# Kernel optimization log

Hardware: AMD Instinct MI355X
Metric: run time of the kernel (lower is better)

## Reference

```python
import jax, jax.numpy as jnp
import numpy as np

N_NODES = 100000
N_EDGES = 1700000  # 1.6M random edges + 100k self-loops (dgl.add_self_loop)
HID = 128
N_GRAPHS = 64
N_CLASSES = 10
T_STEPS = 5


def setup_inputs() -> dict:
    key = jax.random.key(0)
    ks = jax.random.split(key, 12)
    m = jax.random.normal(ks[0], (N_NODES,), dtype=jnp.float32)
    n_rand = N_EDGES - N_NODES
    src_r = jax.random.randint(ks[1], (n_rand,), 0, N_NODES)
    dst_r = jax.random.randint(ks[2], (n_rand,), 0, N_NODES)
    loops = jnp.arange(N_NODES)
    src = jnp.concatenate([src_r, loops])
    dst = jnp.concatenate([dst_r, loops])
    graph_ids = jnp.sort(jax.random.randint(ks[3], (N_NODES,), 0, N_GRAPHS))
    s = 0.05
    W_e = jax.random.normal(ks[4], (HID, HID), dtype=jnp.float32) * s
    b_e = jnp.zeros((HID,), dtype=jnp.float32)
    W_ih = jax.random.normal(ks[5], (3 * HID, HID), dtype=jnp.float32) * s
    b_ih = jnp.zeros((3 * HID,), dtype=jnp.float32)
    W_hh = jax.random.normal(ks[6], (3 * HID, HID), dtype=jnp.float32) * s
    b_hh = jnp.zeros((3 * HID,), dtype=jnp.float32)
    W_cls = jax.random.normal(ks[7], (N_CLASSES, HID), dtype=jnp.float32) * s
    b_cls = jnp.zeros((N_CLASSES,), dtype=jnp.float32)
    return {"m": m, "W_e": W_e, "b_e": b_e, "W_ih": W_ih, "b_ih": b_ih,
            "W_hh": W_hh, "b_hh": b_hh, "W_cls": W_cls, "b_cls": b_cls,
            "src": src, "dst": dst, "graph_ids": graph_ids, "n_graphs": N_GRAPHS}


def _gated_graph_forward(m, W_e, b_e, W_ih, b_ih, W_hh, b_hh, W_cls, b_cls,
                         src, dst, graph_ids, n_graphs):
    n_nodes = m.shape[0]
    hid = W_e.shape[0]
    # h = ndata['m'].view(-1,1), zero-padded to out_feats (DGL GatedGraphConv)
    h = jnp.zeros((n_nodes, hid), dtype=m.dtype).at[:, 0].set(m)
    for _ in range(T_STEPS):
        # single edge type: a[v] = sum_{(u,v) in E} W_e h[u] + b_e
        msg = (h @ W_e.T + b_e)[src]                       # [E, H]
        a = jax.ops.segment_sum(msg, dst, num_segments=n_nodes)
        # torch.nn.GRUCell(a, h); gate order: r, z, n
        gi = a @ W_ih.T + b_ih
        gh = h @ W_hh.T + b_hh
        i_r, i_z, i_n = jnp.split(gi, 3, axis=-1)
        h_r, h_z, h_n = jnp.split(gh, 3, axis=-1)
        r = jax.nn.sigmoid(i_r + h_r)
        z = jax.nn.sigmoid(i_z + h_z)
        n = jnp.tanh(i_n + r * h_n)
        h = (1.0 - z) * n + z * h
    h = jax.nn.relu(h)
    # dgl.mean_nodes: per-graph mean over nodes
    sums = jax.ops.segment_sum(h, graph_ids, num_segments=n_graphs)
    cnt = jax.ops.segment_sum(jnp.ones((n_nodes,), h.dtype), graph_ids,
                              num_segments=n_graphs)
    hg = sums / jnp.maximum(cnt, 1.0)[:, None]             # [G, H]
    return hg @ W_cls.T + b_cls                            # [G, C]


def reference(m, W_e, b_e, W_ih, b_ih, W_hh, b_hh, W_cls, b_cls,
              src, dst, graph_ids, n_graphs):
    return _gated_graph_forward(m, W_e, b_e, W_ih, b_ih, W_hh, b_hh,
                                W_cls, b_cls, src, dst, graph_ids, n_graphs)
```

## Files before the change

kernel.cpp:

```cpp
#include <hip/hip_runtime.h>

#define HID 128
#define G3  384
#define TSTEPS 5
#define BSHIFT 9
#define BNODES (1 << BSHIFT)
#define MAXBUK 256
#define PART_EPB 8192

typedef unsigned int  uint;
typedef unsigned short ushort;

typedef float  f32x4  __attribute__((ext_vector_type(4)));
typedef __bf16 bf16x8 __attribute__((ext_vector_type(8)));

union B8u { uint4 u; bf16x8 b; ushort s[8]; };

static __device__ inline ushort f2bf(float f) {
  uint u = __float_as_uint(f);
  uint r = u + 0x7fffu + ((u >> 16) & 1u);
  return (ushort)(r >> 16);
}
static __device__ inline float bf2f(ushort s) {
  return __uint_as_float(((uint)s) << 16);
}

__global__ __launch_bounds__(128) void k_weights(
    const float* __restrict__ W_e, const float* __restrict__ b_e,
    const float* __restrict__ W_ih, const float* __restrict__ W_hh,
    ushort* __restrict__ Wcomb, ushort* __restrict__ Whh16, float* __restrict__ bvec,
    ushort* __restrict__ Wc0, ushort* __restrict__ Wh0)
{
  int j = blockIdx.x, t = threadIdx.x;
  if (j < G3) {
    __shared__ float row[HID];
    row[t] = W_ih[j * HID + t];
    __syncthreads();
    float acc = 0.f;
    for (int k = 0; k < HID; ++k) acc = fmaf(row[k], W_e[k * HID + t], acc);
    Wcomb[j * HID + t] = f2bf(acc);
    if (t == 0) {
      Wc0[j] = f2bf(acc);
      float b = 0.f;
      for (int k = 0; k < HID; ++k) b += row[k] * b_e[k];
      bvec[j] = b;
    }
  } else {
    int j2 = j - G3;
    Whh16[j2 * HID + t] = f2bf(W_hh[j2 * HID + t]);
    if (t == 0) Wh0[j2] = f2bf(W_hh[j2 * HID]);
  }
}

__global__ __launch_bounds__(256) void k_bh(const int* __restrict__ dst,
                                            int* __restrict__ bhist, int E) {
  __shared__ int lh[MAXBUK];
  int t = threadIdx.x;
  if (t < MAXBUK) lh[t] = 0;
  __syncthreads();
  for (int e = blockIdx.x * 256 + t; e < E; e += gridDim.x * 256)
    atomicAdd(&lh[dst[e] >> BSHIFT], 1);
  __syncthreads();
  if (t < MAXBUK && lh[t]) atomicAdd(&bhist[t], lh[t]);
}

__global__ __launch_bounds__(256) void k_bsc(const int* __restrict__ bhist,
                                             int* __restrict__ bbase,
                                             int* __restrict__ gcur,
                                             int* __restrict__ rowptr, int E, int N) {
  __shared__ int ls[MAXBUK];
  int t = threadIdx.x;
  ls[t] = bhist[t];
  __syncthreads();
  if (t == 0) {
    int run = 0;
    for (int i = 0; i < MAXBUK; ++i) {
      bbase[i] = run; gcur[i] = run; run += ls[i];
    }
    bbase[MAXBUK] = run;
    rowptr[N] = E;
  }
}

__global__ __launch_bounds__(256) void k_part(
    const int* __restrict__ src, const int* __restrict__ dst,
    int* __restrict__ gcur, uint* __restrict__ ebuf, int E) {
  __shared__ int lh[MAXBUK], lbase[MAXBUK], lcur[MAXBUK];
  int t = threadIdx.x;
  int base = blockIdx.x * PART_EPB;
  if (t < MAXBUK) lh[t] = 0;
  __syncthreads();
#pragma unroll 4
  for (int j = 0; j < PART_EPB / 256; ++j) {
    int e = base + j * 256 + t;
    if (e < E) atomicAdd(&lh[dst[e] >> BSHIFT], 1);
  }
  __syncthreads();
  if (t < MAXBUK) {
    lbase[t] = lh[t] ? atomicAdd(&gcur[t], lh[t]) : 0;
    lcur[t] = 0;
  }
  __syncthreads();
#pragma unroll 4
  for (int j = 0; j < PART_EPB / 256; ++j) {
    int e = base + j * 256 + t;
    if (e < E) {
      int d = dst[e];
      int b = d >> BSHIFT;
      int p = atomicAdd(&lcur[b], 1);
      ebuf[lbase[b] + p] = (uint)src[e] | ((uint)(d & (BNODES - 1)) << 20);
    }
  }
}

__global__ __launch_bounds__(256) void k_fill2(
    const uint* __restrict__ ebuf, const int* __restrict__ bbase,
    int* __restrict__ csrc, int* __restrict__ rowptr, int* __restrict__ deg, int N) {
  __shared__ int hcnt[BNODES];
  __shared__ int wls[4];
  int t = threadIdx.x;
  int b = blockIdx.x;
  int ebeg = bbase[b], eend = bbase[b + 1];
  for (int i = t; i < BNODES; i += 256) hcnt[i] = 0;
  __syncthreads();
  for (int e = ebeg + t; e < eend; e += 256)
    atomicAdd(&hcnt[ebuf[e] >> 20], 1);
  __syncthreads();
  const int PER = BNODES / 256;
  int lane = t & 63, wv = t >> 6;
  int x[PER]; int s = 0;
#pragma unroll
  for (int i = 0; i < PER; ++i) { x[i] = hcnt[PER * t + i]; s += x[i]; }
  int incl = s;
#pragma unroll
  for (int off = 1; off < 64; off <<= 1) {
    int u = __shfl_up(incl, off, 64);
    if (lane >= off) incl += u;
  }
  if (lane == 63) wls[wv] = incl;
  __syncthreads();
  int wbase = 0;
  for (int i = 0; i < wv; ++i) wbase += wls[i];
  int run = wbase + incl - s;
#pragma unroll
  for (int i = 0; i < PER; ++i) {
    int node = (b << BSHIFT) + PER * t + i;
    hcnt[PER * t + i] = run;
    if (node < N) { rowptr[node] = ebeg + run; deg[node] = x[i]; }
    run += x[i];
  }
  __syncthreads();
  for (int e = ebeg + t; e < eend; e += 256) {
    uint v = ebuf[e];
    int p = atomicAdd(&hcnt[v >> 20], 1);
    csrc[ebeg + p] = (int)(v & 0xFFFFFu);
  }
}

__global__ void k_minit(const float* __restrict__ m, ushort* __restrict__ m16, int N) {
  int v = blockIdx.x * 256 + threadIdx.x;
  if (v < N) m16[v] = f2bf(m[v]);
}

__global__ __launch_bounds__(256) void k_gather0(
    const int* __restrict__ rowptr, const int* __restrict__ csrc,
    const ushort* __restrict__ m16, ushort* __restrict__ hsum0, int N)
{
  int v = blockIdx.x * 256 + threadIdx.x;
  if (v >= N) return;
  int beg = rowptr[v], end = rowptr[v + 1];
  float a0 = 0.f, a1 = 0.f, a2 = 0.f, a3 = 0.f;
  int e = beg;
  for (; e + 16 <= end; e += 16) {
    a0 += (bf2f(m16[csrc[e + 0]]) + bf2f(m16[csrc[e + 4]])) +
          (bf2f(m16[csrc[e + 8]]) + bf2f(m16[csrc[e + 12]]));
    a1 += (bf2f(m16[csrc[e + 1]]) + bf2f(m16[csrc[e + 5]])) +
          (bf2f(m16[csrc[e + 9]]) + bf2f(m16[csrc[e + 13]]));
    a2 += (bf2f(m16[csrc[e + 2]]) + bf2f(m16[csrc[e + 6]])) +
          (bf2f(m16[csrc[e + 10]]) + bf2f(m16[csrc[e + 14]]));
    a3 += (bf2f(m16[csrc[e + 3]]) + bf2f(m16[csrc[e + 7]])) +
          (bf2f(m16[csrc[e + 11]]) + bf2f(m16[csrc[e + 15]]));
  }
  for (; e < end; e += 4) {
    if (e + 0 < end) a0 += bf2f(m16[csrc[e + 0]]);
    if (e + 1 < end) a1 += bf2f(m16[csrc[e + 1]]);
    if (e + 2 < end) a2 += bf2f(m16[csrc[e + 2]]);
    if (e + 3 < end) a3 += bf2f(m16[csrc[e + 3]]);
  }
  hsum0[v] = f2bf((a0 + a1) + (a2 + a3));
}

__global__ __launch_bounds__(256) void k_gru0(
    const ushort* __restrict__ hsum0, const ushort* __restrict__ m16,
    const int* __restrict__ deg,
    const ushort* __restrict__ Wc0, const ushort* __restrict__ Wh0,
    const float* __restrict__ bvec, const float* __restrict__ b_ih,
    const float* __restrict__ b_hh, ushort* __restrict__ hbn, int N)
{
  int idx = blockIdx.x * 256 + threadIdx.x;
  if (idx >= N * HID) return;
  int n = idx >> 7, d = idx & (HID - 1);
  float s0 = bf2f(hsum0[n]);
  float h0 = bf2f(m16[n]);
  float degf = (float)deg[n];
  float acc0 = s0 * bf2f(Wc0[d]);
  float acc1 = s0 * bf2f(Wc0[d + 128]);
  float acc2 = s0 * bf2f(Wc0[d + 256]);
  float acc3 = h0 * bf2f(Wh0[d]);
  float acc4 = h0 * bf2f(Wh0[d + 128]);
  float acc5 = h0 * bf2f(Wh0[d + 256]);
  float hold = (d == 0) ? h0 : 0.f;
  float ir = acc0 + degf * bvec[d] + b_ih[d];
  float iz = acc1 + degf * bvec[d + 128] + b_ih[d + 128];
  float in_ = acc2 + degf * bvec[d + 256] + b_ih[d + 256];
  float hr = acc3 + b_hh[d];
  float hz = acc4 + b_hh[d + 128];
  float hn = acc5 + b_hh[d + 256];
  float r = __builtin_amdgcn_rcpf(1.f + __expf(-(ir + hr)));
  float z = __builtin_amdgcn_rcpf(1.f + __expf(-(iz + hz)));
  float x2 = in_ + r * hn;
  float e2 = __expf(2.f * x2);
  float nv = 1.f - 2.f * __builtin_amdgcn_rcpf(e2 + 1.f);
  float hv = (1.f - z) * nv + z * hold;
  hbn[idx] = f2bf(hv);
}

static __device__ __forceinline__ void gather_strip(
    const int* __restrict__ rowptr, const int* __restrict__ csrc,
    const ushort* __restrict__ hb, const int* __restrict__ deg,
    int strip, int w, int lane, int N,
    ushort dstS[16][128], ushort dstH[16][128], int* dstDeg)
{
  int node = strip * 16 + w;
  if (node >= N) return;
  int g = lane >> 4;
  int i = lane & 15;
  if (g == 1)
    *(uint4*)(&dstH[w][(i ^ (w & 7)) * 8]) =
        *(const uint4*)(hb + (size_t)node * HID + i * 8);
  if (lane == 32) dstDeg[w] = deg[node];
  int beg = rowptr[node], end = rowptr[node + 1];
  float acc[8] = {0.f, 0.f, 0.f, 0.f, 0.f, 0.f, 0.f, 0.f};
  int e = beg;
  for (; e + 16 <= end; e += 16) {
    int s0 = csrc[e + g];
    int s1 = csrc[e + 4 + g];
    int s2 = csrc[e + 8 + g];
    int s3 = csrc[e + 12 + g];
    B8u w0; w0.u = *(const uint4*)(hb + (size_t)s0 * HID + i * 8);
    B8u w1; w1.u = *(const uint4*)(hb + (size_t)s1 * HID + i * 8);
    B8u w2; w2.u = *(const uint4*)(hb + (size_t)s2 * HID + i * 8);
    B8u w3; w3.u = *(const uint4*)(hb + (size_t)s3 * HID + i * 8);
#pragma unroll
    for (int j = 0; j < 8; ++j)
      acc[j] += (bf2f(w0.s[j]) + bf2f(w1.s[j])) + (bf2f(w2.s[j]) + bf2f(w3.s[j]));
  }
  int rem = end - e;
  if (rem > 0) {
    int t0 = (g < rem)      ? csrc[e + g]      : -1;
    int t1 = (4 + g < rem)  ? csrc[e + 4 + g]  : -1;
    int t2 = (8 + g < rem)  ? csrc[e + 8 + g]  : -1;
    int t3 = (12 + g < rem) ? csrc[e + 12 + g] : -1;
    B8u r0, r1, r2, r3;
    if (t0 >= 0) r0.u = *(const uint4*)(hb + (size_t)t0 * HID + i * 8);
    if (t1 >= 0) r1.u = *(const uint4*)(hb + (size_t)t1 * HID + i * 8);
    if (t2 >= 0) r2.u = *(const uint4*)(hb + (size_t)t2 * HID + i * 8);
    if (t3 >= 0) r3.u = *(const uint4*)(hb + (size_t)t3 * HID + i * 8);
    if (t0 >= 0) {
#pragma unroll
      for (int j = 0; j < 8; ++j) acc[j] += bf2f(r0.s[j]);
    }
    if (t1 >= 0) {
#pragma unroll
      for (int j = 0; j < 8; ++j) acc[j] += bf2f(r1.s[j]);
    }
    if (t2 >= 0) {
#pragma unroll
      for (int j = 0; j < 8; ++j) acc[j] += bf2f(r2.s[j]);
    }
    if (t3 >= 0) {
#pragma unroll
      for (int j = 0; j < 8; ++j) acc[j] += bf2f(r3.s[j]);
    }
  }
#pragma unroll
  for (int j = 0; j < 8; ++j) {
    acc[j] += __shfl_xor(acc[j], 16, 64);
    acc[j] += __shfl_xor(acc[j], 32, 64);
  }
  if (g == 0) {
    uint4 ov;
    ov.x = ((uint)f2bf(acc[1]) << 16) | (uint)f2bf(acc[0]);
    ov.y = ((uint)f2bf(acc[3]) << 16) | (uint)f2bf(acc[2]);
    ov.z = ((uint)f2bf(acc[5]) << 16) | (uint)f2bf(acc[4]);
    ov.w = ((uint)f2bf(acc[7]) << 16) | (uint)f2bf(acc[6]);
    *(uint4*)(&dstS[w][(i ^ (w & 7)) * 8]) = ov;
  }
}

__global__ __launch_bounds__(1024, 4) void k_fused(
    const int* __restrict__ rowptr, const int* __restrict__ csrc,
    const ushort* __restrict__ hbc, ushort* __restrict__ hbn,
    const ushort* __restrict__ Wcomb, const ushort* __restrict__ Whh16,
    const float* __restrict__ bvec, const float* __restrict__ b_ih,
    const float* __restrict__ b_hh, const int* __restrict__ deg, int N)
{
  __shared__ float S[6][16][132];
  __shared__ ushort AT[3][2][16][128];
  __shared__ int degT[3][16];
  const int tid = threadIdx.x;
  const int w = tid >> 6;
  const int lane = tid & 63;
  const int quad = lane >> 4, l16 = lane & 15;
  const int gm = w >> 3;
  const int gw = w & 7;
  const int d0 = gw * 16;

  const ushort* Wmat = gm ? Whh16 : Wcomb;
  B8u bfr[3][4];
#pragma unroll
  for (int g = 0; g < 3; ++g)
#pragma unroll
    for (int kc = 0; kc < 4; ++kc) {
      int j = (d0 + g * 128 + l16) * HID + kc * 32 + quad * 8;
      bfr[g][kc].u = *(const uint4*)(Wmat + j);
    }

  const int ecol = tid & 127, erow0 = tid >> 7;
  const float bir = b_ih[ecol], biz = b_ih[ecol + 128], bin_ = b_ih[ecol + 256];
  const float bhr = b_hh[ecol], bhz = b_hh[ecol + 128], bhn = b_hh[ecol + 256];
  const float vr = bvec[ecol], vz = bvec[ecol + 128], vn = bvec[ecol + 256];

  const int nstrip = N >> 4;
  const int G = (int)gridDim.x;
  int s = blockIdx.x;
  if (s >= nstrip) return;

  gather_strip(rowptr, csrc, hbc, deg, s, w, lane, N, AT[0][0], AT[0][1], degT[0]);
  asm volatile("s_waitcnt lgkmcnt(0)" ::: "memory");
  __builtin_amdgcn_sched_barrier(0);
  __builtin_amdgcn_s_barrier();

  int cur = 0;
  while (true) {
    int ns = s + G;
    bool more = ns < nstrip;
    int nxt = (cur == 2) ? 0 : cur + 1;
    if (more)
      gather_strip(rowptr, csrc, hbc, deg, ns, w, lane, N,
                   AT[nxt][0], AT[nxt][1], degT[nxt]);
    B8u af[4];
#pragma unroll
    for (int kc = 0; kc < 4; ++kc)
      af[kc].u = *(const uint4*)(&AT[cur][gm][l16][(((quad + 4 * kc) ^ (l16 & 7)) * 8)]);
    f32x4 acc[3] = {};
#pragma unroll
    for (int kc = 0; kc < 4; ++kc)
#pragma unroll
      for (int g = 0; g < 3; ++g)
        acc[g] = __builtin_amdgcn_mfma_f32_16x16x32_bf16(af[kc].b, bfr[g][kc].b, acc[g], 0, 0, 0);
    __builtin_amdgcn_s_barrier();
#pragma unroll
    for (int g = 0; g < 3; ++g)
#pragma unroll
      for (int rg = 0; rg < 4; ++rg)
        S[gm * 3 + g][quad * 4 + rg][d0 + l16] = acc[g][rg];
    asm volatile("s_waitcnt lgkmcnt(0)" ::: "memory");
    __builtin_amdgcn_sched_barrier(0);
    __builtin_amdgcn_s_barrier();
    int n0 = s << 4;
#pragma unroll
    for (int k = 0; k < 2; ++k) {
      int row = erow0 + 8 * k;
      float dgf = (float)degT[cur][row];
      int sc = (((ecol >> 3) ^ (row & 7)) * 8) + (ecol & 7);
      float hold = bf2f(AT[cur][1][row][sc]);
      float ir  = S[0][row][ecol] + dgf * vr + bir;
      float iz  = S[1][row][ecol] + dgf * vz + biz;
      float in_ = S[2][row][ecol] + dgf * vn + bin_;
      float hr  = S[3][row][ecol] + bhr;
      float hz  = S[4][row][ecol] + bhz;
      float hn  = S[5][row][ecol] + bhn;
      float r = __builtin_amdgcn_rcpf(1.f + __expf(-(ir + hr)));
      float z = __builtin_amdgcn_rcpf(1.f + __expf(-(iz + hz)));
      float x2 = in_ + r * hn;
      float e2 = __expf(2.f * x2);
      float nv = 1.f - 2.f * __builtin_amdgcn_rcpf(e2 + 1.f);
      float hv = (1.f - z) * nv + z * hold;
      hbn[(size_t)(n0 + row) * HID + ecol] = f2bf(hv);
    }
    if (!more) break;
    s = ns; cur = nxt;
  }
}

__global__ __launch_bounds__(64) void k_bounds(const int* __restrict__ gid,
                                               int* __restrict__ cnt, int N, int G) {
  int g = threadIdx.x;
  if (g >= G) return;
  int lo = 0, hi = N;
  while (lo < hi) { int mid = (lo + hi) >> 1; if (gid[mid] < g) lo = mid + 1; else hi = mid; }
  int lb0 = lo;
  lo = 0; hi = N;
  int g1 = g + 1;
  while (lo < hi) { int mid = (lo + hi) >> 1; if (gid[mid] < g1) lo = mid + 1; else hi = mid; }
  cnt[g] = lo - lb0;
}

#define POOL_CHUNK 96
__global__ __launch_bounds__(128) void k_pool(const ushort* __restrict__ hb,
                                              const int* __restrict__ gid,
                                              float* __restrict__ hg, int N) {
  int d = threadIdx.x;
  int start = blockIdx.x * POOL_CHUNK;
  if (start >= N) return;
  int end = min(start + POOL_CHUNK, N);
  float acc = 0.f;
  int g = gid[start];
  for (int n = start; n < end; ++n) {
    int gn = gid[n];
    if (gn != g) { unsafeAtomicAdd(&hg[g * HID + d], acc); acc = 0.f; g = gn; }
    acc += fmaxf(bf2f(hb[(size_t)n * HID + d]), 0.f);
  }
  unsafeAtomicAdd(&hg[g * HID + d], acc);
}

__global__ __launch_bounds__(640) void k_cls(const float* __restrict__ hg,
                                             const int* __restrict__ cnt,
                                             const float* __restrict__ Wc,
                                             const float* __restrict__ bc,
                                             float* __restrict__ out, int G) {
  int t = threadIdx.x;
  if (t >= G * 10) return;
  int g = t / 10, c = t % 10;
  float inv = 1.f / fmaxf((float)cnt[g], 1.f);
  float acc = 0.f;
  for (int d = 0; d < HID; ++d) acc = fmaf(hg[g * HID + d], Wc[c * HID + d], acc);
  out[t] = acc * inv + bc[c];
}

extern "C" void kernel_launch(void* const* d_in, const int* in_sizes, int n_in,
                              void* d_out, int out_size, void* d_ws, size_t ws_size,
                              hipStream_t stream) {
  const int N = in_sizes[0];
  const int E = in_sizes[9];
  const float* m    = (const float*)d_in[0];
  const float* W_e  = (const float*)d_in[1];
  const float* b_e  = (const float*)d_in[2];
  const float* W_ih = (const float*)d_in[3];
  const float* b_ih = (const float*)d_in[4];
  const float* W_hh = (const float*)d_in[5];
  const float* b_hh = (const float*)d_in[6];
  const float* W_cls = (const float*)d_in[7];
  const float* b_cls = (const float*)d_in[8];
  const int* src = (const int*)d_in[9];
  const int* dst = (const int*)d_in[10];
  const int* gid = (const int*)d_in[11];
  const int G = out_size / 10;
  float* out = (float*)d_out;

  size_t off = 0;
  auto alloc = [&](size_t b) {
    char* p = (char*)d_ws + off;
    off += (b + 255) & ~(size_t)255;
    return (void*)p;
  };
  ushort* hb0    = (ushort*)alloc((size_t)N * HID * 2);
  ushort* hb1    = (ushort*)alloc((size_t)N * HID * 2);
  int*    deg    = (int*)   alloc((size_t)N * 4);
  int*    rowptr = (int*)   alloc((size_t)(N + 1) * 4);
  int*    csrc   = (int*)   alloc((size_t)E * 4);
  uint*   ebuf   = (uint*)  alloc((size_t)E * 4);
  int*    bhist  = (int*)   alloc((size_t)MAXBUK * 4);
  int*    bbase  = (int*)   alloc((size_t)(MAXBUK + 1) * 4);
  int*    gcur   = (int*)   alloc((size_t)MAXBUK * 4);
  ushort* Wcomb  = (ushort*)alloc((size_t)G3 * HID * 2);
  ushort* Whh16  = (ushort*)alloc((size_t)G3 * HID * 2);
  float*  bvec   = (float*) alloc((size_t)G3 * 4);
  float*  hg     = (float*) alloc((size_t)G * HID * 4);
  int*    cnt    = (int*)   alloc((size_t)G * 4);
  ushort* m16    = (ushort*)alloc((size_t)N * 2);
  ushort* hsum0  = (ushort*)alloc((size_t)N * 2);
  ushort* Wc0    = (ushort*)alloc((size_t)G3 * 2);
  ushort* Wh0    = (ushort*)alloc((size_t)G3 * 2);
  if (off > ws_size) return;

  const int NBUK = (N + BNODES - 1) >> BSHIFT;

  k_weights<<<2 * G3, HID, 0, stream>>>(W_e, b_e, W_ih, W_hh, Wcomb, Whh16, bvec, Wc0, Wh0);
  k_minit<<<(N + 255) / 256, 256, 0, stream>>>(m, m16, N);
  hipMemsetAsync(bhist, 0, (size_t)MAXBUK * 4, stream);
  k_bh<<<256, 256, 0, stream>>>(dst, bhist, E);
  k_bsc<<<1, MAXBUK, 0, stream>>>(bhist, bbase, gcur, rowptr, E, N);
  k_part<<<(E + PART_EPB - 1) / PART_EPB, 256, 0, stream>>>(src, dst, gcur, ebuf, E);
  k_fill2<<<NBUK, 256, 0, stream>>>(ebuf, bbase, csrc, rowptr, deg, N);

  k_gather0<<<(N + 255) / 256, 256, 0, stream>>>(rowptr, csrc, m16, hsum0, N);
  k_gru0<<<(N * HID + 255) / 256, 256, 0, stream>>>(hsum0, m16, deg, Wc0, Wh0,
                                                    bvec, b_ih, b_hh, hb1, N);

  ushort* hbc = hb1;
  ushort* hbn = hb0;
  const int nstrip = N >> 4;
  const int fuse_blocks = nstrip < 256 ? nstrip : 256;
  for (int s = 1; s < TSTEPS; ++s) {
    k_fused<<<fuse_blocks, 1024, 0, stream>>>(rowptr, csrc, hbc, hbn,
                                              Wcomb, Whh16, bvec, b_ih, b_hh, deg, N);
    ushort* t = hbc; hbc = hbn; hbn = t;
  }

  hipMemsetAsync(hg, 0, (size_t)G * HID * 4, stream);
  k_bounds<<<1, 64, 0, stream>>>(gid, cnt, N, G);
  k_pool<<<(N + POOL_CHUNK - 1) / POOL_CHUNK, HID, 0, stream>>>(hbc, gid, hg, N);
  k_cls<<<1, 640, 0, stream>>>(hg, cnt, W_cls, b_cls, out, G);
}
```

Measured before the change: 764.6 us.

## Prefetch neighbor indices one strip ahead and specialize gather for low degree

The fused GRU kernel now loads the CSR neighbor indices (up to 28 per node) for the strip after next while the current strip is processed. This breaks the dependent load chain rowptr→csrc→h row inside the gather. Nodes with up to 28 edges take an unrolled path that issues all row loads at once, and higher-degree nodes fall back to the generic loop. Bias vectors are moved into shared memory to free registers, at the cost of holding seven more index registers per lane under a 1024-thread launch bound.

```diff
diff --git a/kernel.cpp b/kernel.cpp
--- a/kernel.cpp
+++ b/kernel.cpp
@@ -225,6 +225,54 @@
   hbn[idx] = f2bf(hv);
 }
 
+static __device__ __forceinline__ void accum_range(
+    const ushort* __restrict__ hb, const int* __restrict__ csrc,
+    int beg, int end, int g, int i, float acc[8])
+{
+  int e = beg;
+  for (; e + 16 <= end; e += 16) {
+    int s0 = csrc[e + g];
+    int s1 = csrc[e + 4 + g];
+    int s2 = csrc[e + 8 + g];
+    int s3 = csrc[e + 12 + g];
+    B8u w0; w0.u = *(const uint4*)(hb + (size_t)s0 * HID + i * 8);
+    B8u w1; w1.u = *(const uint4*)(hb + (size_t)s1 * HID + i * 8);
+    B8u w2; w2.u = *(const uint4*)(hb + (size_t)s2 * HID + i * 8);
+    B8u w3; w3.u = *(const uint4*)(hb + (size_t)s3 * HID + i * 8);
+#pragma unroll
+    for (int j = 0; j < 8; ++j)
+      acc[j] += (bf2f(w0.s[j]) + bf2f(w1.s[j])) + (bf2f(w2.s[j]) + bf2f(w3.s[j]));
+  }
+  int rem = end - e;
+  if (rem > 0) {
+    int t0 = (g < rem)      ? csrc[e + g]      : -1;
+    int t1 = (4 + g < rem)  ? csrc[e + 4 + g]  : -1;
+    int t2 = (8 + g < rem)  ? csrc[e + 8 + g]  : -1;
+    int t3 = (12 + g < rem) ? csrc[e + 12 + g] : -1;
+    B8u r0, r1, r2, r3;
+    if (t0 >= 0) r0.u = *(const uint4*)(hb + (size_t)t0 * HID + i * 8);
+    if (t1 >= 0) r1.u = *(const uint4*)(hb + (size_t)t1 * HID + i * 8);
+    if (t2 >= 0) r2.u = *(const uint4*)(hb + (size_t)t2 * HID + i * 8);
+    if (t3 >= 0) r3.u = *(const uint4*)(hb + (size_t)t3 * HID + i * 8);
+    if (t0 >= 0) {
+#pragma unroll
+      for (int j = 0; j < 8; ++j) acc[j] += bf2f(r0.s[j]);
+    }
+    if (t1 >= 0) {
+#pragma unroll
+      for (int j = 0; j < 8; ++j) acc[j] += bf2f(r1.s[j]);
+    }
+    if (t2 >= 0) {
+#pragma unroll
+      for (int j = 0; j < 8; ++j) acc[j] += bf2f(r2.s[j]);
+    }
+    if (t3 >= 0) {
+#pragma unroll
+      for (int j = 0; j < 8; ++j) acc[j] += bf2f(r3.s[j]);
+    }
+  }
+}
+
 static __device__ __forceinline__ void gather_strip(
     const int* __restrict__ rowptr, const int* __restrict__ csrc,
     const ushort* __restrict__ hb, const int* __restrict__ deg,
@@ -241,48 +289,7 @@
   if (lane == 32) dstDeg[w] = deg[node];
   int beg = rowptr[node], end = rowptr[node + 1];
   float acc[8] = {0.f, 0.f, 0.f, 0.f, 0.f, 0.f, 0.f, 0.f};
-  int e = beg;
-  for (; e + 16 <= end; e += 16) {
-    int s0 = csrc[e + g];
-    int s1 = csrc[e + 4 + g];
-    int s2 = csrc[e + 8 + g];
-    int s3 = csrc[e + 12 + g];
-    B8u w0; w0.u = *(const uint4*)(hb + (size_t)s0 * HID + i * 8);
-    B8u w1; w1.u = *(const uint4*)(hb + (size_t)s1 * HID + i * 8);
-    B8u w2; w2.u = *(const uint4*)(hb + (size_t)s2 * HID + i * 8);
-    B8u w3; w3.u = *(const uint4*)(hb + (size_t)s3 * HID + i * 8);
-#pragma unroll
-    for (int j = 0; j < 8; ++j)
-      acc[j] += (bf2f(w0.s[j]) + bf2f(w1.s[j])) + (bf2f(w2.s[j]) + bf2f(w3.s[j]));
-  }
-  int rem = end - e;
-  if (rem > 0) {
-    int t0 = (g < rem)      ? csrc[e + g]      : -1;
-    int t1 = (4 + g < rem)  ? csrc[e + 4 + g]  : -1;
-    int t2 = (8 + g < rem)  ? csrc[e + 8 + g]  : -1;
-    int t3 = (12 + g < rem) ? csrc[e + 12 + g] : -1;
-    B8u r0, r1, r2, r3;
-    if (t0 >= 0) r0.u = *(const uint4*)(hb + (size_t)t0 * HID + i * 8);
-    if (t1 >= 0) r1.u = *(const uint4*)(hb + (size_t)t1 * HID + i * 8);
-    if (t2 >= 0) r2.u = *(const uint4*)(hb + (size_t)t2 * HID + i * 8);
-    if (t3 >= 0) r3.u = *(const uint4*)(hb + (size_t)t3 * HID + i * 8);
-    if (t0 >= 0) {
-#pragma unroll
-      for (int j = 0; j < 8; ++j) acc[j] += bf2f(r0.s[j]);
-    }
-    if (t1 >= 0) {
-#pragma unroll
-      for (int j = 0; j < 8; ++j) acc[j] += bf2f(r1.s[j]);
-    }
-    if (t2 >= 0) {
-#pragma unroll
-      for (int j = 0; j < 8; ++j) acc[j] += bf2f(r2.s[j]);
-    }
-    if (t3 >= 0) {
-#pragma unroll
-      for (int j = 0; j < 8; ++j) acc[j] += bf2f(r3.s[j]);
-    }
-  }
+  accum_range(hb, csrc, beg, end, g, i, acc);
 #pragma unroll
   for (int j = 0; j < 8; ++j) {
     acc[j] += __shfl_xor(acc[j], 16, 64);
@@ -308,6 +315,7 @@
   __shared__ float S[6][16][132];
   __shared__ ushort AT[3][2][16][128];
   __shared__ int degT[3][16];
+  __shared__ float BL[9][128];
   const int tid = threadIdx.x;
   const int w = tid >> 6;
   const int lane = tid & 63;
@@ -319,24 +327,37 @@
   const ushort* Wmat = gm ? Whh16 : Wcomb;
   B8u bfr[3][4];
 #pragma unroll
-  for (int g = 0; g < 3; ++g)
+  for (int gg = 0; gg < 3; ++gg)
 #pragma unroll
     for (int kc = 0; kc < 4; ++kc) {
-      int j = (d0 + g * 128 + l16) * HID + kc * 32 + quad * 8;
-      bfr[g][kc].u = *(const uint4*)(Wmat + j);
-    }
+      int j = (d0 + gg * 128 + l16) * HID + kc * 32 + quad * 8;
+      bfr[gg][kc].u = *(const uint4*)(Wmat + j);
+    }
+
+  for (int kk = tid; kk < 9 * 128; kk += 1024) {
+    int grp = kk >> 7, col = kk & 127;
+    const float* sp2 = (grp < 3) ? b_ih : (grp < 6 ? b_hh : bvec);
+    BL[grp][col] = sp2[(grp % 3) * 128 + col];
+  }
 
   const int ecol = tid & 127, erow0 = tid >> 7;
-  const float bir = b_ih[ecol], biz = b_ih[ecol + 128], bin_ = b_ih[ecol + 256];
-  const float bhr = b_hh[ecol], bhz = b_hh[ecol + 128], bhn = b_hh[ecol + 256];
-  const float vr = bvec[ecol], vz = bvec[ecol + 128], vn = bvec[ecol + 256];
-
   const int nstrip = N >> 4;
   const int G = (int)gridDim.x;
   int s = blockIdx.x;
   if (s >= nstrip) return;
 
   gather_strip(rowptr, csrc, hbc, deg, s, w, lane, N, AT[0][0], AT[0][1], degT[0]);
+  int cnt = 0; int idx[7];
+#pragma unroll
+  for (int j = 0; j < 7; ++j) idx[j] = 0;
+  if (s + G < nstrip) {
+    int node = (s + G) * 16 + w;
+    int b2 = rowptr[node];
+    cnt = rowptr[node + 1] - b2;
+#pragma unroll
+    for (int j = 0; j < 7; ++j)
+      idx[j] = (4 * j + quad < cnt) ? csrc[b2 + 4 * j + quad] : 0;
+  }
   asm volatile("s_waitcnt lgkmcnt(0)" ::: "memory");
   __builtin_amdgcn_sched_barrier(0);
   __builtin_amdgcn_s_barrier();
@@ -346,48 +367,144 @@
     int ns = s + G;
     bool more = ns < nstrip;
     int nxt = (cur == 2) ? 0 : cur + 1;
-    if (more)
-      gather_strip(rowptr, csrc, hbc, deg, ns, w, lane, N,
-                   AT[nxt][0], AT[nxt][1], degT[nxt]);
+    if (more) {
+      int node = ns * 16 + w;
+      int s2 = ns + G;
+      int nbeg = 0, nend = 0;
+      if (s2 < nstrip) {
+        int node2 = s2 * 16 + w;
+        nbeg = rowptr[node2];
+        nend = rowptr[node2 + 1];
+      }
+      uint4 hrow = make_uint4(0, 0, 0, 0);
+      if (quad == 1) hrow = *(const uint4*)(hbc + (size_t)node * HID + l16 * 8);
+      int dgv = 0;
+      if (lane == 32) dgv = deg[node];
+      float acc[8] = {0.f, 0.f, 0.f, 0.f, 0.f, 0.f, 0.f, 0.f};
+      if (cnt > 28) {
+        int beg = rowptr[node];
+        accum_range(hbc, csrc, beg, beg + cnt, quad, l16, acc);
+      } else {
+        bool h16 = cnt >= 16;
+        bool p0 = (quad < cnt), p1 = (4 + quad < cnt),
+             p2 = (8 + quad < cnt), p3 = (12 + quad < cnt);
+        bool p4 = (16 + quad < cnt), p5 = (20 + quad < cnt), p6 = (24 + quad < cnt);
+        B8u r0, r1, r2, r3, t4, t5, t6;
+        if (h16) {
+          r0.u = *(const uint4*)(hbc + (size_t)idx[0] * HID + l16 * 8);
+          r1.u = *(const uint4*)(hbc + (size_t)idx[1] * HID + l16 * 8);
+          r2.u = *(const uint4*)(hbc + (size_t)idx[2] * HID + l16 * 8);
+          r3.u = *(const uint4*)(hbc + (size_t)idx[3] * HID + l16 * 8);
+        } else {
+          if (p0) r0.u = *(const uint4*)(hbc + (size_t)idx[0] * HID + l16 * 8);
+          if (p1) r1.u = *(const uint4*)(hbc + (size_t)idx[1] * HID + l16 * 8);
+          if (p2) r2.u = *(const uint4*)(hbc + (size_t)idx[2] * HID + l16 * 8);
+          if (p3) r3.u = *(const uint4*)(hbc + (size_t)idx[3] * HID + l16 * 8);
+        }
+        if (p4) t4.u = *(const uint4*)(hbc + (size_t)idx[4] * HID + l16 * 8);
+        if (p5) t5.u = *(const uint4*)(hbc + (size_t)idx[5] * HID + l16 * 8);
+        if (p6) t6.u = *(const uint4*)(hbc + (size_t)idx[6] * HID + l16 * 8);
+        if (h16) {
+#pragma unroll
+          for (int j = 0; j < 8; ++j)
+            acc[j] += (bf2f(r0.s[j]) + bf2f(r1.s[j])) + (bf2f(r2.s[j]) + bf2f(r3.s[j]));
+        } else {
+          if (p0) {
+#pragma unroll
+            for (int j = 0; j < 8; ++j) acc[j] += bf2f(r0.s[j]);
+          }
+          if (p1) {
+#pragma unroll
+            for (int j = 0; j < 8; ++j) acc[j] += bf2f(r1.s[j]);
+          }
+          if (p2) {
+#pragma unroll
+            for (int j = 0; j < 8; ++j) acc[j] += bf2f(r2.s[j]);
+          }
+          if (p3) {
+#pragma unroll
+            for (int j = 0; j < 8; ++j) acc[j] += bf2f(r3.s[j]);
+          }
+        }
+        if (p4) {
+#pragma unroll
+          for (int j = 0; j < 8; ++j) acc[j] += bf2f(t4.s[j]);
+        }
+        if (p5) {
+#pragma unroll
+          for (int j = 0; j < 8; ++j) acc[j] += bf2f(t5.s[j]);
+        }
+        if (p6) {
+#pragma unroll
+          for (int j = 0; j < 8; ++j) acc[j] += bf2f(t6.s[j]);
+        }
+      }
+#pragma unroll
+      for (int j = 0; j < 8; ++j) {
+        acc[j] += __shfl_xor(acc[j], 16, 64);
+        acc[j] += __shfl_xor(acc[j], 32, 64);
+      }
+      if (quad == 0) {
+        uint4 ov;
+        ov.x = ((uint)f2bf(acc[1]) << 16) | (uint)f2bf(acc[0]);
+        ov.y = ((uint)f2bf(acc[3]) << 16) | (uint)f2bf(acc[2]);
+        ov.z = ((uint)f2bf(acc[5]) << 16) | (uint)f2bf(acc[4]);
+        ov.w = ((uint)f2bf(acc[7]) << 16) | (uint)f2bf(acc[6]);
+        *(uint4*)(&AT[nxt][0][w][(l16 ^ (w & 7)) * 8]) = ov;
+      }
+      if (quad == 1) *(uint4*)(&AT[nxt][1][w][(l16 ^ (w & 7)) * 8]) = hrow;
+      if (lane == 32) degT[nxt][w] = dgv;
+      if (s2 < nstrip) {
+        cnt = nend - nbeg;
+#pragma unroll
+        for (int j = 0; j < 7; ++j)
+          idx[j] = (4 * j + quad < cnt) ? csrc[nbeg + 4 * j + quad] : 0;
+      } else cnt = 0;
+    }
     B8u af[4];
 #pragma unroll
     for (int kc = 0; kc < 4; ++kc)
       af[kc].u = *(const uint4*)(&AT[cur][gm][l16][(((quad + 4 * kc) ^ (l16 & 7)) * 8)]);
-    f32x4 acc[3] = {};
+    f32x4 acc3[3] = {};
 #pragma unroll
     for (int kc = 0; kc < 4; ++kc)
 #pragma unroll
-      for (int g = 0; g < 3; ++g)
-        acc[g] = __builtin_amdgcn_mfma_f32_16x16x32_bf16(af[kc].b, bfr[g][kc].b, acc[g], 0, 0, 0);
+      for (int gg = 0; gg < 3; ++gg)
+        acc3[gg] = __builtin_amdgcn_mfma_f32_16x16x32_bf16(af[kc].b, bfr[gg][kc].b, acc3[gg], 0, 0, 0);
     __builtin_amdgcn_s_barrier();
 #pragma unroll
-    for (int g = 0; g < 3; ++g)
+    for (int gg = 0; gg < 3; ++gg)
 #pragma unroll
       for (int rg = 0; rg < 4; ++rg)
-        S[gm * 3 + g][quad * 4 + rg][d0 + l16] = acc[g][rg];
+        S[gm * 3 + gg][quad * 4 + rg][d0 + l16] = acc3[gg][rg];
     asm volatile("s_waitcnt lgkmcnt(0)" ::: "memory");
     __builtin_amdgcn_sched_barrier(0);
     __builtin_amdgcn_s_barrier();
-    int n0 = s << 4;
-#pragma unroll
-    for (int k = 0; k < 2; ++k) {
-      int row = erow0 + 8 * k;
-      float dgf = (float)degT[cur][row];
-      int sc = (((ecol >> 3) ^ (row & 7)) * 8) + (ecol & 7);
-      float hold = bf2f(AT[cur][1][row][sc]);
-      float ir  = S[0][row][ecol] + dgf * vr + bir;
-      float iz  = S[1][row][ecol] + dgf * vz + biz;
-      float in_ = S[2][row][ecol] + dgf * vn + bin_;
-      float hr  = S[3][row][ecol] + bhr;
-      float hz  = S[4][row][ecol] + bhz;
-      float hn  = S[5][row][ecol] + bhn;
-      float r = __builtin_amdgcn_rcpf(1.f + __expf(-(ir + hr)));
-      float z = __builtin_amdgcn_rcpf(1.f + __expf(-(iz + hz)));
-      float x2 = in_ + r * hn;
-      float e2 = __expf(2.f * x2);
-      float nv = 1.f - 2.f * __builtin_amdgcn_rcpf(e2 + 1.f);
-      float hv = (1.f - z) * nv + z * hold;
-      hbn[(size_t)(n0 + row) * HID + ecol] = f2bf(hv);
+    {
+      float bir = BL[0][ecol], biz = BL[1][ecol], bin_ = BL[2][ecol];
+      float bhr = BL[3][ecol], bhz = BL[4][ecol], bhn = BL[5][ecol];
+      float vr = BL[6][ecol], vz = BL[7][ecol], vn = BL[8][ecol];
+      int n0 = s << 4;
+#pragma unroll
+      for (int k = 0; k < 2; ++k) {
+        int row = erow0 + 8 * k;
+        float dgf = (float)degT[cur][row];
+        int sc = (((ecol >> 3) ^ (row & 7)) * 8) + (ecol & 7);
+        float hold = bf2f(AT[cur][1][row][sc]);
+        float ir  = S[0][row][ecol] + dgf * vr + bir;
+        float iz  = S[1][row][ecol] + dgf * vz + biz;
+        float in_ = S[2][row][ecol] + dgf * vn + bin_;
+        float hr  = S[3][row][ecol] + bhr;
+        float hz  = S[4][row][ecol] + bhz;
+        float hn  = S[5][row][ecol] + bhn;
+        float r = __builtin_amdgcn_rcpf(1.f + __expf(-(ir + hr)));
+        float z = __builtin_amdgcn_rcpf(1.f + __expf(-(iz + hz)));
+        float x2 = in_ + r * hn;
+        float e2 = __expf(2.f * x2);
+        float nv = 1.f - 2.f * __builtin_amdgcn_rcpf(e2 + 1.f);
+        float hv = (1.f - z) * nv + z * hold;
+        hbn[(size_t)(n0 + row) * HID + ecol] = f2bf(hv);
+      }
     }
     if (!more) break;
     s = ns; cur = nxt;
```

Result: slower. 1.301 ms (+70.2%).

## Sort nodes by in-degree so each fused strip has uniform gather work

Applied to the files above, without the earlier changes.

Adds a degree histogram, scan and scatter that build a permutation of nodes ordered by in-degree, with per-slot edge begin offset and degree. The fused GRU kernel walks strips in this sorted order and writes results back through the original node index. The aim is to cut load imbalance between the 16 waves of a strip, where one high-degree node stalls the block barrier. In exchange it adds three small preprocessing kernels and an indirection, and it makes the reads of old h and the output writes scattered rather than contiguous.

```diff
diff --git a/kernel.cpp b/kernel.cpp
--- a/kernel.cpp
+++ b/kernel.cpp
@@ -7,6 +7,7 @@
 #define BNODES (1 << BSHIFT)
 #define MAXBUK 256
 #define PART_EPB 8192
+#define DBUK 64
 
 typedef unsigned int  uint;
 typedef unsigned short ushort;
@@ -155,6 +156,39 @@
     int p = atomicAdd(&hcnt[v >> 20], 1);
     csrc[ebeg + p] = (int)(v & 0xFFFFFu);
   }
+}
+
+__global__ __launch_bounds__(256) void k_dhist(const int* __restrict__ deg,
+                                               int* __restrict__ dhist, int N) {
+  __shared__ int lh[DBUK];
+  int t = threadIdx.x;
+  if (t < DBUK) lh[t] = 0;
+  __syncthreads();
+  for (int v = blockIdx.x * 256 + t; v < N; v += gridDim.x * 256)
+    atomicAdd(&lh[min(deg[v], DBUK - 1)], 1);
+  __syncthreads();
+  if (t < DBUK && lh[t]) atomicAdd(&dhist[t], lh[t]);
+}
+
+__global__ __launch_bounds__(64) void k_dscan(const int* __restrict__ dhist,
+                                              int* __restrict__ dcur) {
+  if (threadIdx.x == 0) {
+    int run = 0;
+    for (int i = 0; i < DBUK; ++i) { dcur[i] = run; run += dhist[i]; }
+  }
+}
+
+__global__ __launch_bounds__(256) void k_dscatter(
+    const int* __restrict__ deg, const int* __restrict__ rowptr,
+    int* __restrict__ dcur, int* __restrict__ orig2,
+    int* __restrict__ beg2, int* __restrict__ deg2s, int N) {
+  int v = blockIdx.x * 256 + threadIdx.x;
+  if (v >= N) return;
+  int d = deg[v];
+  int k = atomicAdd(&dcur[min(d, DBUK - 1)], 1);
+  orig2[k] = v;
+  beg2[k] = rowptr[v];
+  deg2s[k] = d;
 }
 
 __global__ void k_minit(const float* __restrict__ m, ushort* __restrict__ m16, int N) {
@@ -225,22 +259,10 @@
   hbn[idx] = f2bf(hv);
 }
 
-static __device__ __forceinline__ void gather_strip(
-    const int* __restrict__ rowptr, const int* __restrict__ csrc,
-    const ushort* __restrict__ hb, const int* __restrict__ deg,
-    int strip, int w, int lane, int N,
-    ushort dstS[16][128], ushort dstH[16][128], int* dstDeg)
+static __device__ __forceinline__ void accum_range(
+    const ushort* __restrict__ hb, const int* __restrict__ csrc,
+    int beg, int end, int g, int i, float acc[8])
 {
-  int node = strip * 16 + w;
-  if (node >= N) return;
-  int g = lane >> 4;
-  int i = lane & 15;
-  if (g == 1)
-    *(uint4*)(&dstH[w][(i ^ (w & 7)) * 8]) =
-        *(const uint4*)(hb + (size_t)node * HID + i * 8);
-  if (lane == 32) dstDeg[w] = deg[node];
-  int beg = rowptr[node], end = rowptr[node + 1];
-  float acc[8] = {0.f, 0.f, 0.f, 0.f, 0.f, 0.f, 0.f, 0.f};
   int e = beg;
   for (; e + 16 <= end; e += 16) {
     int s0 = csrc[e + g];
@@ -283,6 +305,29 @@
       for (int j = 0; j < 8; ++j) acc[j] += bf2f(r3.s[j]);
     }
   }
+}
+
+static __device__ __forceinline__ void gather_strip_sorted(
+    const int* __restrict__ beg2, const int* __restrict__ deg2s,
+    const int* __restrict__ orig2, const int* __restrict__ csrc,
+    const ushort* __restrict__ hb,
+    int strip, int w, int lane, int N,
+    ushort dstS[16][128], ushort dstH[16][128], int* dstDeg, int* dstOrig)
+{
+  int k = strip * 16 + w;
+  if (k >= N) return;
+  int g = lane >> 4;
+  int i = lane & 15;
+  int orig = orig2[k];
+  int beg = beg2[k];
+  int cnt = deg2s[k];
+  if (g == 1)
+    *(uint4*)(&dstH[w][(i ^ (w & 7)) * 8]) =
+        *(const uint4*)(hb + (size_t)orig * HID + i * 8);
+  if (lane == 0) dstOrig[w] = orig;
+  if (lane == 32) dstDeg[w] = cnt;
+  float acc[8] = {0.f, 0.f, 0.f, 0.f, 0.f, 0.f, 0.f, 0.f};
+  accum_range(hb, csrc, beg, beg + cnt, g, i, acc);
 #pragma unroll
   for (int j = 0; j < 8; ++j) {
     acc[j] += __shfl_xor(acc[j], 16, 64);
@@ -299,15 +344,17 @@
 }
 
 __global__ __launch_bounds__(1024, 4) void k_fused(
-    const int* __restrict__ rowptr, const int* __restrict__ csrc,
+    const int* __restrict__ beg2, const int* __restrict__ deg2s,
+    const int* __restrict__ orig2, const int* __restrict__ csrc,
     const ushort* __restrict__ hbc, ushort* __restrict__ hbn,
     const ushort* __restrict__ Wcomb, const ushort* __restrict__ Whh16,
     const float* __restrict__ bvec, const float* __restrict__ b_ih,
-    const float* __restrict__ b_hh, const int* __restrict__ deg, int N)
+    const float* __restrict__ b_hh, int N)
 {
   __shared__ float S[6][16][132];
   __shared__ ushort AT[3][2][16][128];
   __shared__ int degT[3][16];
+  __shared__ int origT[3][16];
   const int tid = threadIdx.x;
   const int w = tid >> 6;
   const int lane = tid & 63;
@@ -336,7 +383,8 @@
   int s = blockIdx.x;
   if (s >= nstrip) return;
 
-  gather_strip(rowptr, csrc, hbc, deg, s, w, lane, N, AT[0][0], AT[0][1], degT[0]);
+  gather_strip_sorted(beg2, deg2s, orig2, csrc, hbc, s, w, lane, N,
+                      AT[0][0], AT[0][1], degT[0], origT[0]);
   asm volatile("s_waitcnt lgkmcnt(0)" ::: "memory");
   __builtin_amdgcn_sched_barrier(0);
   __builtin_amdgcn_s_barrier();
@@ -347,8 +395,8 @@
     bool more = ns < nstrip;
     int nxt = (cur == 2) ? 0 : cur + 1;
     if (more)
-      gather_strip(rowptr, csrc, hbc, deg, ns, w, lane, N,
-                   AT[nxt][0], AT[nxt][1], degT[nxt]);
+      gather_strip_sorted(beg2, deg2s, orig2, csrc, hbc, ns, w, lane, N,
+                          AT[nxt][0], AT[nxt][1], degT[nxt], origT[nxt]);
     B8u af[4];
 #pragma unroll
     for (int kc = 0; kc < 4; ++kc)
@@ -373,6 +421,7 @@
     for (int k = 0; k < 2; ++k) {
       int row = erow0 + 8 * k;
       float dgf = (float)degT[cur][row];
+      int og = origT[cur][row];
       int sc = (((ecol >> 3) ^ (row & 7)) * 8) + (ecol & 7);
       float hold = bf2f(AT[cur][1][row][sc]);
       float ir  = S[0][row][ecol] + dgf * vr + bir;
@@ -387,7 +436,8 @@
       float e2 = __expf(2.f * x2);
       float nv = 1.f - 2.f * __builtin_amdgcn_rcpf(e2 + 1.f);
       float hv = (1.f - z) * nv + z * hold;
-      hbn[(size_t)(n0 + row) * HID + ecol] = f2bf(hv);
+      if (n0 + row < N)
+        hbn[(size_t)og * HID + ecol] = f2bf(hv);
     }
     if (!more) break;
     s = ns; cur = nxt;
@@ -483,6 +533,11 @@
   ushort* hsum0  = (ushort*)alloc((size_t)N * 2);
   ushort* Wc0    = (ushort*)alloc((size_t)G3 * 2);
   ushort* Wh0    = (ushort*)alloc((size_t)G3 * 2);
+  int*    dhist  = (int*)   alloc((size_t)DBUK * 4);
+  int*    dcur   = (int*)   alloc((size_t)DBUK * 4);
+  int*    orig2  = (int*)   alloc((size_t)N * 4);
+  int*    beg2   = (int*)   alloc((size_t)N * 4);
+  int*    deg2s  = (int*)   alloc((size_t)N * 4);
   if (off > ws_size) return;
 
   const int NBUK = (N + BNODES - 1) >> BSHIFT;
@@ -495,6 +550,11 @@
   k_part<<<(E + PART_EPB - 1) / PART_EPB, 256, 0, stream>>>(src, dst, gcur, ebuf, E);
   k_fill2<<<NBUK, 256, 0, stream>>>(ebuf, bbase, csrc, rowptr, deg, N);
 
+  hipMemsetAsync(dhist, 0, (size_t)DBUK * 4, stream);
+  k_dhist<<<64, 256, 0, stream>>>(deg, dhist, N);
+  k_dscan<<<1, 64, 0, stream>>>(dhist, dcur);
+  k_dscatter<<<(N + 255) / 256, 256, 0, stream>>>(deg, rowptr, dcur, orig2, beg2, deg2s, N);
+
   k_gather0<<<(N + 255) / 256, 256, 0, stream>>>(rowptr, csrc, m16, hsum0, N);
   k_gru0<<<(N * HID + 255) / 256, 256, 0, stream>>>(hsum0, m16, deg, Wc0, Wh0,
                                                     bvec, b_ih, b_hh, hb1, N);
@@ -504,8 +564,8 @@
   const int nstrip = N >> 4;
   const int fuse_blocks = nstrip < 256 ? nstrip : 256;
   for (int s = 1; s < TSTEPS; ++s) {
-    k_fused<<<fuse_blocks, 1024, 0, stream>>>(rowptr, csrc, hbc, hbn,
-                                              Wcomb, Whh16, bvec, b_ih, b_hh, deg, N);
+    k_fused<<<fuse_blocks, 1024, 0, stream>>>(beg2, deg2s, orig2, csrc, hbc, hbn,
+                                              Wcomb, Whh16, bvec, b_ih, b_hh, N);
     ushort* t = hbc; hbc = hbn; hbn = t;
   }
 
```

New measurement: 1.025 ms. +34.1%, slower.
